# Kernel tuning notes

Measured on AMD Instinct MI355X. Metric: run time of the kernel, lower is better.

## Reference

```python
import jax, jax.numpy as jnp
import numpy as np

D_MODEL = 512
N_HEAD = 8
D_FF = 2048
HEAD = D_MODEL // N_HEAD
B, S = 2, 4096
LN_EPS = 1e-5


def _layernorm(x, g, b):
    mu = jnp.mean(x, axis=-1, keepdims=True)
    var = jnp.mean(jnp.square(x - mu), axis=-1, keepdims=True)
    return (x - mu) * jax.lax.rsqrt(var + LN_EPS) * g + b


def setup_inputs() -> dict:
    key = jax.random.key(0)
    ks = jax.random.split(key, 12)
    s = 0.02
    inp = {
        "src": jax.random.normal(ks[0], (B, S, D_MODEL), dtype=jnp.float32),
        "mask": jnp.ones((B, S, S), dtype=jnp.float32),
        "Wq": jax.random.normal(ks[1], (D_MODEL, D_MODEL), dtype=jnp.float32) * s,
        "bq": jnp.zeros((D_MODEL,), dtype=jnp.float32),
        "Wk": jax.random.normal(ks[2], (D_MODEL, D_MODEL), dtype=jnp.float32) * s,
        "bk": jnp.zeros((D_MODEL,), dtype=jnp.float32),
        "Wv": jax.random.normal(ks[3], (D_MODEL, D_MODEL), dtype=jnp.float32) * s,
        "bv": jnp.zeros((D_MODEL,), dtype=jnp.float32),
        "Wo": jax.random.normal(ks[4], (D_MODEL, D_MODEL), dtype=jnp.float32) * s,
        "bo": jnp.zeros((D_MODEL,), dtype=jnp.float32),
        "W1": jax.random.normal(ks[5], (D_FF, D_MODEL), dtype=jnp.float32) * s,
        "b1": jnp.zeros((D_FF,), dtype=jnp.float32),
        "W2": jax.random.normal(ks[6], (D_MODEL, D_FF), dtype=jnp.float32) * s,
        "b2": jnp.zeros((D_MODEL,), dtype=jnp.float32),
        "ln1_g": jnp.ones((D_MODEL,), dtype=jnp.float32),
        "ln1_b": jnp.zeros((D_MODEL,), dtype=jnp.float32),
        "ln2_g": jnp.ones((D_MODEL,), dtype=jnp.float32),
        "ln2_b": jnp.zeros((D_MODEL,), dtype=jnp.float32),
    }
    return inp


def reference(src, mask, Wq, bq, Wk, bk, Wv, bv, Wo, bo, W1, b1, W2, b2,
              ln1_g, ln1_b, ln2_g, ln2_b):
    # --- multi-head self-attention (chunk/cat == head split on last dim) ---
    def heads(x, W, b):
        y = x @ W.T + b  # [B,S,D]
        return y.reshape(B, S, N_HEAD, HEAD)
    Q = heads(src, Wq, bq)
    K = heads(src, Wk, bk)
    V = heads(src, Wv, bv)
    score = jnp.einsum('bihd,bjhd->bhij', Q, K) / jnp.sqrt(jnp.float32(HEAD))
    score = score + ((1.0 - mask) * -1e9)[:, None, :, :]
    attn = jax.nn.softmax(score, axis=-1)
    ctx = jnp.einsum('bhij,bjhd->bihd', attn, V).reshape(B, S, D_MODEL)
    sa = ctx @ Wo.T + bo
    # --- residual + LN1 ---
    x = _layernorm(src + sa, ln1_g, ln1_b)
    # --- FFN (relu) + residual + LN2 ---
    ff = jax.nn.relu(x @ W1.T + b1) @ W2.T + b2
    return _layernorm(x + ff, ln2_g, ln2_b)
```

## Files before the change

### kernel.cpp

```cpp
#include <hip/hip_runtime.h>
#include <cstdint>
#include <cstddef>

#define DM   512
#define SQL  4096
#define NHE  8
#define HDM  64
#define DFF  2048
#define NB   2

typedef unsigned short u16t;
typedef __attribute__((ext_vector_type(8))) __bf16 bf16x8;
typedef __attribute__((ext_vector_type(4))) float f32x4;
typedef __attribute__((ext_vector_type(8))) unsigned short us8;
typedef __attribute__((ext_vector_type(4))) unsigned short us4;

__device__ inline f32x4 mfma16(bf16x8 a, bf16x8 b, f32x4 c) {
    return __builtin_amdgcn_mfma_f32_16x16x32_bf16(a, b, c, 0, 0, 0);
}

__device__ inline void load_lds16(const void* g, void* l) {
    __builtin_amdgcn_global_load_lds(
        (const __attribute__((address_space(1))) unsigned int*)g,
        (__attribute__((address_space(3))) unsigned int*)l, 16, 0, 0);
}

__device__ inline u16t f2bf(float x) {
    union { float f; unsigned int u; } v; v.f = x;
    unsigned int r = v.u + 0x7fffu + ((v.u >> 16) & 1u);
    return (u16t)(r >> 16);
}

__device__ inline void store_out(float* C, size_t idx, float v) { C[idx] = v; }
__device__ inline void store_out(u16t* C, size_t idx, float v) { C[idx] = f2bf(v); }

__global__ __launch_bounds__(256) void convert_all(
    const float* __restrict__ src, const float* __restrict__ Wq,
    const float* __restrict__ Wk, const float* __restrict__ Wv,
    const float* __restrict__ Wo, const float* __restrict__ W1,
    const float* __restrict__ W2, const float* __restrict__ bq,
    const float* __restrict__ bk, const float* __restrict__ bv,
    u16t* __restrict__ srcbf, u16t* __restrict__ wqkv, u16t* __restrict__ woc,
    u16t* __restrict__ w1c, u16t* __restrict__ w2c,
    float* __restrict__ bqkv, int* __restrict__ flag) {
    const int blk = blockIdx.x;
    const float* s;
    u16t* d;
    int base;
    if (blk < 2048)      { s = src; d = srcbf;           base = blk; }
    else if (blk < 2176) { s = Wq;  d = wqkv;            base = blk - 2048; }
    else if (blk < 2304) { s = Wk;  d = wqkv + 262144;   base = blk - 2176; }
    else if (blk < 2432) { s = Wv;  d = wqkv + 524288;   base = blk - 2304; }
    else if (blk < 2560) { s = Wo;  d = woc;             base = blk - 2432; }
    else if (blk < 3072) { s = W1;  d = w1c;             base = blk - 2560; }
    else if (blk < 3584) { s = W2;  d = w2c;             base = blk - 3072; }
    else {
        for (int i = threadIdx.x; i < 1536; i += 256)
            bqkv[i] = (i < 512) ? bq[i] : (i < 1024 ? bk[i - 512] : bv[i - 1024]);
        if (threadIdx.x == 0) flag[0] = 1;
        return;
    }
    const int i = base * 2048 + threadIdx.x * 8;
    f32x4 a = *(const f32x4*)(s + i);
    f32x4 b = *(const f32x4*)(s + i + 4);
    us8 o;
    o[0] = f2bf(a[0]); o[1] = f2bf(a[1]); o[2] = f2bf(a[2]); o[3] = f2bf(a[3]);
    o[4] = f2bf(b[0]); o[5] = f2bf(b[1]); o[6] = f2bf(b[2]); o[7] = f2bf(b[3]);
    *(us8*)(d + i) = o;
}

__global__ __launch_bounds__(256) void check_mask_k(const f32x4* __restrict__ m, int* flag) {
    const size_t n4 = (size_t)NB * SQL * SQL / 4;
    size_t i = (size_t)blockIdx.x * 256 + threadIdx.x;
    bool bad = false;
    for (; i < n4; i += (size_t)gridDim.x * 256) {
        f32x4 v = m[i];
        bad |= (v[0] != 1.0f) || (v[1] != 1.0f) || (v[2] != 1.0f) || (v[3] != 1.0f);
    }
    if (bad) flag[0] = 0;
}

template <typename OutT, bool RELU>
__global__ __launch_bounds__(256, 3) void gemm_bt(const u16t* __restrict__ A,
                                                  const u16t* __restrict__ Bw,
                                                  const float* __restrict__ bias,
                                                  OutT* __restrict__ C,
                                                  const int M, const int N, const int K,
                                                  const int ldc) {
    __shared__ u16t As[128 * 32];
    __shared__ u16t Bs[128 * 32];
    const int tid = threadIdx.x;
    const int w = tid >> 6, lane = tid & 63;
    const int l15 = lane & 15, quad = lane >> 4;
    const int m0 = blockIdx.y * 128, n0 = blockIdx.x * 128;
    const int wm = w >> 1, wn = w & 1;

    f32x4 acc[4][4] = {};

    const u16t* Ag = A + ((size_t)(m0 + w * 32 + (lane >> 2))) * K + (lane & 3) * 8;
    const u16t* Bg = Bw + ((size_t)(n0 + w * 32 + (lane >> 2))) * K + (lane & 3) * 8;
    u16t* Asw = &As[(w * 32) * 32];
    u16t* Bsw = &Bs[(w * 32) * 32];

    for (int k0 = 0; k0 < K; k0 += 32) {
        __syncthreads();
        load_lds16(Ag + k0, Asw);
        load_lds16(Ag + (size_t)16 * K + k0, Asw + 16 * 32);
        load_lds16(Bg + k0, Bsw);
        load_lds16(Bg + (size_t)16 * K + k0, Bsw + 16 * 32);
        __syncthreads();
        bf16x8 af[4], bfr[4];
#pragma unroll
        for (int mt = 0; mt < 4; ++mt)
            af[mt] = *(const bf16x8*)&As[(wm * 64 + mt * 16 + l15) * 32 + quad * 8];
#pragma unroll
        for (int nt = 0; nt < 4; ++nt)
            bfr[nt] = *(const bf16x8*)&Bs[(wn * 64 + nt * 16 + l15) * 32 + quad * 8];
#pragma unroll
        for (int mt = 0; mt < 4; ++mt)
#pragma unroll
            for (int nt = 0; nt < 4; ++nt)
                acc[mt][nt] = mfma16(af[mt], bfr[nt], acc[mt][nt]);
    }

    float bv[4];
#pragma unroll
    for (int nt = 0; nt < 4; ++nt) bv[nt] = bias[n0 + wn * 64 + nt * 16 + l15];
#pragma unroll
    for (int mt = 0; mt < 4; ++mt)
#pragma unroll
        for (int r = 0; r < 4; ++r) {
            const int row = m0 + wm * 64 + mt * 16 + quad * 4 + r;
#pragma unroll
            for (int nt = 0; nt < 4; ++nt) {
                float v = acc[mt][nt][r] + bv[nt];
                if (RELU) v = fmaxf(v, 0.0f);
                store_out(C, (size_t)row * ldc + n0 + wn * 64 + nt * 16 + l15, v);
            }
        }
}

__global__ __launch_bounds__(256) void transpose_v(const u16t* __restrict__ qkv,
                                                   u16t* __restrict__ vt) {
    __shared__ u16t t[64 * 72];
    const int sb = blockIdx.x, h = blockIdx.y, b = blockIdx.z;
    const int tid = threadIdx.x;
#pragma unroll
    for (int it = 0; it < 2; ++it) {
        const int idx = it * 256 + tid;
        const int r = idx >> 3, c8 = idx & 7;
        const u16t* gp = qkv + (size_t)(b * SQL + sb * 64 + r) * (3 * DM) + 2 * DM + h * HDM + c8 * 8;
        *(us8*)&t[r * 72 + c8 * 8] = *(const us8*)gp;
    }
    __syncthreads();
#pragma unroll
    for (int it = 0; it < 2; ++it) {
        const int idx = it * 256 + tid;
        const int d = idx >> 3, s8 = idx & 7;
        us8 o;
#pragma unroll
        for (int u = 0; u < 8; ++u) o[u] = t[(s8 * 8 + u) * 72 + d];
        u16t* gp = vt + (size_t)((b * NHE + h) * HDM + d) * SQL + sb * 64 + s8 * 8;
        *(us8*)gp = o;
    }
}

__global__ __launch_bounds__(256, 2) void flash_attn(const u16t* __restrict__ qkv,
                                                     const u16t* __restrict__ vtg,
                                                     const float* __restrict__ mask,
                                                     const int* __restrict__ flag,
                                                     u16t* __restrict__ ctx) {
    __shared__ u16t Ks[128 * 64];
    __shared__ u16t Vs[64 * 128];
    __shared__ u16t Ps[4][32 * 128];

    const int qt = blockIdx.x, h = blockIdx.y, b = blockIdx.z;
    const int tid = threadIdx.x;
    const int w = tid >> 6, lane = tid & 63;
    const int l15 = lane & 15, quad = lane >> 4;
    const int e3 = l15 & 7;
    const bool allones = (*flag != 0);

    bf16x8 qf[2][2];
#pragma unroll
    for (int mt = 0; mt < 2; ++mt) {
        const size_t rowb = (size_t)(b * SQL + qt * 128 + w * 32 + mt * 16 + l15) * (3 * DM) + h * HDM;
#pragma unroll
        for (int kk = 0; kk < 2; ++kk)
            qf[mt][kk] = *(const bf16x8*)(qkv + rowb + kk * 32 + quad * 8);
    }

    f32x4 oacc[4][2] = {};
    float m_r[2] = {-3.0e38f, -3.0e38f};
    float l_r[2] = {0.0f, 0.0f};

    const int r8 = lane >> 3, c8 = lane & 7;
    const int r4 = lane >> 4, c16 = lane & 15;

    for (int kt = 0; kt < SQL / 128; ++kt) {
        const int j0 = kt * 128;
        __syncthreads();
#pragma unroll
        for (int i = 0; i < 4; ++i) {
            const int row = j0 + w * 32 + i * 8 + r8;
            load_lds16(qkv + (size_t)(b * SQL + row) * (3 * DM) + DM + h * HDM + ((c8 ^ r8) * 8),
                       &Ks[(w * 32 + i * 8) * 64]);
        }
#pragma unroll
        for (int i = 0; i < 4; ++i) {
            const int d = w * 16 + i * 4 + r4;
            load_lds16(vtg + (size_t)((b * NHE + h) * HDM + d) * SQL + j0 + ((c16 ^ ((i * 4 + r4) & 7)) * 8),
                       &Vs[(w * 16 + i * 4) * 128]);
        }
        __syncthreads();

        f32x4 sacc[2][8] = {};
#pragma unroll
        for (int kk = 0; kk < 2; ++kk) {
#pragma unroll
            for (int jt = 0; jt < 8; ++jt) {
                bf16x8 af = *(const bf16x8*)&Ks[(jt * 16 + l15) * 64 + (((kk * 4 + quad) ^ e3) * 8)];
                sacc[0][jt] = mfma16(af, qf[0][kk], sacc[0][jt]);
                sacc[1][jt] = mfma16(af, qf[1][kk], sacc[1][jt]);
            }
        }

#pragma unroll
        for (int mt = 0; mt < 2; ++mt) {
            float mx = -3.0e38f;
            if (allones) {
#pragma unroll
                for (int jt = 0; jt < 8; ++jt)
#pragma unroll
                    for (int r = 0; r < 4; ++r) {
                        const float v = sacc[mt][jt][r] * 0.125f;
                        sacc[mt][jt][r] = v;
                        mx = fmaxf(mx, v);
                    }
            } else {
                const int gi = qt * 128 + w * 32 + mt * 16 + l15;
#pragma unroll
                for (int jt = 0; jt < 8; ++jt)
#pragma unroll
                    for (int r = 0; r < 4; ++r) {
                        const int gj = j0 + jt * 16 + quad * 4 + r;
                        const float v = sacc[mt][jt][r] * 0.125f
                                      + (1.0f - mask[((size_t)b * SQL + gi) * SQL + gj]) * (-1.0e9f);
                        sacc[mt][jt][r] = v;
                        mx = fmaxf(mx, v);
                    }
            }
            mx = fmaxf(mx, __shfl_xor(mx, 16));
            mx = fmaxf(mx, __shfl_xor(mx, 32));
            const float mnew = fmaxf(m_r[mt], mx);
            const float alpha = __expf(m_r[mt] - mnew);
            m_r[mt] = mnew;
            float rsum = 0.0f;
#pragma unroll
            for (int jt = 0; jt < 8; ++jt) {
                us4 pk;
#pragma unroll
                for (int r = 0; r < 4; ++r) {
                    const float p = __expf(sacc[mt][jt][r] - mnew);
                    rsum += p;
                    pk[r] = f2bf(p);
                }
                *(us4*)&Ps[w][(mt * 16 + l15) * 128
                              + (((jt * 2 + (quad >> 1)) ^ e3) * 8) + (quad & 1) * 4] = pk;
            }
            rsum += __shfl_xor(rsum, 16);
            rsum += __shfl_xor(rsum, 32);
            l_r[mt] = l_r[mt] * alpha + rsum;
#pragma unroll
            for (int dt = 0; dt < 4; ++dt)
#pragma unroll
                for (int r = 0; r < 4; ++r) oacc[dt][mt][r] *= alpha;
        }

#pragma unroll
        for (int ks = 0; ks < 4; ++ks) {
            const int pc = ((ks * 4 + quad) ^ e3) * 8;
            bf16x8 pb0 = *(const bf16x8*)&Ps[w][(l15) * 128 + pc];
            bf16x8 pb1 = *(const bf16x8*)&Ps[w][(16 + l15) * 128 + pc];
#pragma unroll
            for (int dt = 0; dt < 4; ++dt) {
                bf16x8 av = *(const bf16x8*)&Vs[(dt * 16 + l15) * 128 + pc];
                oacc[dt][0] = mfma16(av, pb0, oacc[dt][0]);
                oacc[dt][1] = mfma16(av, pb1, oacc[dt][1]);
            }
        }
    }

#pragma unroll
    for (int mt = 0; mt < 2; ++mt) {
        const float inv = 1.0f / l_r[mt];
        const int token = qt * 128 + w * 32 + mt * 16 + l15;
#pragma unroll
        for (int dt = 0; dt < 4; ++dt) {
            us4 o;
#pragma unroll
            for (int r = 0; r < 4; ++r) o[r] = f2bf(oacc[dt][mt][r] * inv);
            *(us4*)&ctx[(size_t)(b * SQL + token) * DM + h * HDM + dt * 16 + quad * 4] = o;
        }
    }
}

template <bool WBF>
__global__ __launch_bounds__(256) void ln_fused(const float* __restrict__ xa,
                                                const float* __restrict__ xb,
                                                const float* __restrict__ g,
                                                const float* __restrict__ be,
                                                float* __restrict__ outf,
                                                u16t* __restrict__ outh) {
    const int row = blockIdx.x * 4 + (threadIdx.x >> 6);
    const int lane = threadIdx.x & 63;
    const size_t base = (size_t)row * DM;
    f32x4 a0 = *(const f32x4*)(xa + base + lane * 4);
    f32x4 b0 = *(const f32x4*)(xb + base + lane * 4);
    f32x4 a1 = *(const f32x4*)(xa + base + 256 + lane * 4);
    f32x4 b1 = *(const f32x4*)(xb + base + 256 + lane * 4);
    f32x4 v0 = a0 + b0, v1 = a1 + b1;
    float s = v0[0] + v0[1] + v0[2] + v0[3] + v1[0] + v1[1] + v1[2] + v1[3];
    float q = v0[0]*v0[0] + v0[1]*v0[1] + v0[2]*v0[2] + v0[3]*v0[3]
            + v1[0]*v1[0] + v1[1]*v1[1] + v1[2]*v1[2] + v1[3]*v1[3];
#pragma unroll
    for (int off = 1; off < 64; off <<= 1) {
        s += __shfl_xor(s, off);
        q += __shfl_xor(q, off);
    }
    const float mean = s * (1.0f / DM);
    const float var = q * (1.0f / DM) - mean * mean;
    const float rs = rsqrtf(var + 1e-5f);
    f32x4 g0 = *(const f32x4*)(g + lane * 4);
    f32x4 g1 = *(const f32x4*)(g + 256 + lane * 4);
    f32x4 e0 = *(const f32x4*)(be + lane * 4);
    f32x4 e1 = *(const f32x4*)(be + 256 + lane * 4);
    f32x4 y0, y1;
#pragma unroll
    for (int i = 0; i < 4; ++i) {
        y0[i] = (v0[i] - mean) * rs * g0[i] + e0[i];
        y1[i] = (v1[i] - mean) * rs * g1[i] + e1[i];
    }
    *(f32x4*)(outf + base + lane * 4) = y0;
    *(f32x4*)(outf + base + 256 + lane * 4) = y1;
    if (WBF) {
        us4 h0, h1;
#pragma unroll
        for (int i = 0; i < 4; ++i) { h0[i] = f2bf(y0[i]); h1[i] = f2bf(y1[i]); }
        *(us4*)(outh + base + lane * 4) = h0;
        *(us4*)(outh + base + 256 + lane * 4) = h1;
    }
}

extern "C" void kernel_launch(void* const* d_in, const int* in_sizes, int n_in,
                              void* d_out, int out_size, void* d_ws, size_t ws_size,
                              hipStream_t stream) {
    const float* src  = (const float*)d_in[0];
    const float* mask = (const float*)d_in[1];
    const float* Wq = (const float*)d_in[2];
    const float* bq = (const float*)d_in[3];
    const float* Wk = (const float*)d_in[4];
    const float* bk = (const float*)d_in[5];
    const float* Wv = (const float*)d_in[6];
    const float* bv = (const float*)d_in[7];
    const float* Wo = (const float*)d_in[8];
    const float* bo = (const float*)d_in[9];
    const float* W1 = (const float*)d_in[10];
    const float* b1 = (const float*)d_in[11];
    const float* W2 = (const float*)d_in[12];
    const float* b2 = (const float*)d_in[13];
    const float* ln1g = (const float*)d_in[14];
    const float* ln1b = (const float*)d_in[15];
    const float* ln2g = (const float*)d_in[16];
    const float* ln2b = (const float*)d_in[17];

    const int M = NB * SQL;

    char* p = (char*)d_ws;
    auto take = [&](size_t bytes) {
        char* r = p;
        p += (bytes + 1023) & ~(size_t)1023;
        return r;
    };
    u16t* regA   = (u16t*)take((size_t)M * DFF * 2);
    u16t* vtb    = (u16t*)take((size_t)NB * NHE * HDM * SQL * 2);
    u16t* ctxb   = (u16t*)take((size_t)M * DM * 2);
    float* sa_ff = (float*)take((size_t)M * DM * 4);
    float* x1f   = (float*)take((size_t)M * DM * 4);
    u16t* x1h    = (u16t*)take((size_t)M * DM * 2);
    u16t* srcbf  = (u16t*)take((size_t)M * DM * 2);
    u16t* wqkv   = (u16t*)take((size_t)3 * DM * DM * 2);
    float* bqkv  = (float*)take((size_t)3 * DM * 4);
    u16t* woc    = (u16t*)take((size_t)DM * DM * 2);
    u16t* w1c    = (u16t*)take((size_t)DFF * DM * 2);
    u16t* w2c    = (u16t*)take((size_t)DM * DFF * 2);
    int* flag    = (int*)take(1024);
    u16t* qkvb   = regA;
    u16t* hbuf   = regA;

    convert_all<<<3585, 256, 0, stream>>>(src, Wq, Wk, Wv, Wo, W1, W2, bq, bk, bv,
                                          srcbf, wqkv, woc, w1c, w2c, bqkv, flag);
    check_mask_k<<<4096, 256, 0, stream>>>((const f32x4*)mask, flag);

    gemm_bt<u16t, false><<<dim3(12, 64), 256, 0, stream>>>(srcbf, wqkv, bqkv, qkvb,
                                                           M, 3 * DM, DM, 3 * DM);
    transpose_v<<<dim3(SQL / 64, NHE, NB), 256, 0, stream>>>(qkvb, vtb);
    flash_attn<<<dim3(SQL / 128, NHE, NB), 256, 0, stream>>>(qkvb, vtb, mask, flag, ctxb);
    gemm_bt<float, false><<<dim3(4, 64), 256, 0, stream>>>(ctxb, woc, bo, sa_ff,
                                                           M, DM, DM, DM);
    ln_fused<true><<<M / 4, 256, 0, stream>>>(src, sa_ff, ln1g, ln1b, x1f, x1h);
    gemm_bt<u16t, true><<<dim3(16, 64), 256, 0, stream>>>(x1h, w1c, b1, hbuf,
                                                          M, DFF, DM, DFF);
    gemm_bt<float, false><<<dim3(4, 64), 256, 0, stream>>>(hbuf, w2c, b2, sa_ff,
                                                           M, DM, DFF, DM);
    ln_fused<false><<<M / 4, 256, 0, stream>>>(x1f, sa_ff, ln2g, ln2b, (float*)d_out,
                                               (u16t*)nullptr);
}
```

Measured before the change: 497.2 us.

## Keep softmax probabilities in registers and feed PV MFMA directly, drop LDS P buffer

The attention kernel no longer writes the bf16 probabilities to a per-wave LDS scratch and reads them back. The S accumulator layout is reused directly as the A operand of a 16x16x16 bf16 MFMA, with V and O roles transposed and per-row alpha and l values redistributed by shuffles. Dropping the P buffer frees LDS so occupancy is raised to 4 blocks per CU, and the scale and exp are folded into a single exp2 with a premultiplied constant. In exchange the PV product uses the narrower K=16 MFMA (twice as many instructions), the output stores become scalar 2-byte writes, and the higher occupancy target may cause register spills.

Measured after the change: 738.4 us. 1.49x slower.

```diff
diff --git a/kernel.cpp b/kernel.cpp
--- a/kernel.cpp
+++ b/kernel.cpp
@@ -14,9 +14,13 @@
 typedef __attribute__((ext_vector_type(4))) float f32x4;
 typedef __attribute__((ext_vector_type(8))) unsigned short us8;
 typedef __attribute__((ext_vector_type(4))) unsigned short us4;
+typedef __attribute__((ext_vector_type(4))) short s16x4;
 
 __device__ inline f32x4 mfma16(bf16x8 a, bf16x8 b, f32x4 c) {
     return __builtin_amdgcn_mfma_f32_16x16x32_bf16(a, b, c, 0, 0, 0);
+}
+__device__ inline f32x4 mfma16k16(s16x4 a, s16x4 b, f32x4 c) {
+    return __builtin_amdgcn_mfma_f32_16x16x16bf16_1k(a, b, c, 0, 0, 0);
 }
 
 __device__ inline void load_lds16(const void* g, void* l) {
@@ -165,14 +169,13 @@
     }
 }
 
-__global__ __launch_bounds__(256, 2) void flash_attn(const u16t* __restrict__ qkv,
+__global__ __launch_bounds__(256, 4) void flash_attn(const u16t* __restrict__ qkv,
                                                      const u16t* __restrict__ vtg,
                                                      const float* __restrict__ mask,
                                                      const int* __restrict__ flag,
                                                      u16t* __restrict__ ctx) {
     __shared__ u16t Ks[128 * 64];
     __shared__ u16t Vs[64 * 128];
-    __shared__ u16t Ps[4][32 * 128];
 
     const int qt = blockIdx.x, h = blockIdx.y, b = blockIdx.z;
     const int tid = threadIdx.x;
@@ -225,82 +228,83 @@
             }
         }
 
+        float av[2][4];
 #pragma unroll
         for (int mt = 0; mt < 2; ++mt) {
-            float mx = -3.0e38f;
-            if (allones) {
-#pragma unroll
-                for (int jt = 0; jt < 8; ++jt)
-#pragma unroll
-                    for (int r = 0; r < 4; ++r) {
-                        const float v = sacc[mt][jt][r] * 0.125f;
-                        sacc[mt][jt][r] = v;
-                        mx = fmaxf(mx, v);
-                    }
-            } else {
+            if (!allones) {
                 const int gi = qt * 128 + w * 32 + mt * 16 + l15;
 #pragma unroll
                 for (int jt = 0; jt < 8; ++jt)
 #pragma unroll
                     for (int r = 0; r < 4; ++r) {
                         const int gj = j0 + jt * 16 + quad * 4 + r;
-                        const float v = sacc[mt][jt][r] * 0.125f
-                                      + (1.0f - mask[((size_t)b * SQL + gi) * SQL + gj]) * (-1.0e9f);
-                        sacc[mt][jt][r] = v;
-                        mx = fmaxf(mx, v);
+                        sacc[mt][jt][r] = sacc[mt][jt][r] * 0.125f
+                                        + (1.0f - mask[((size_t)b * SQL + gi) * SQL + gj]) * (-1.0e9f);
                     }
             }
+            float mx = -3.0e38f;
+#pragma unroll
+            for (int jt = 0; jt < 8; ++jt)
+#pragma unroll
+                for (int r = 0; r < 4; ++r) mx = fmaxf(mx, sacc[mt][jt][r]);
             mx = fmaxf(mx, __shfl_xor(mx, 16));
             mx = fmaxf(mx, __shfl_xor(mx, 32));
+            const float cs = allones ? 0.18033688011112042f : 1.4426950408889634f;
             const float mnew = fmaxf(m_r[mt], mx);
-            const float alpha = __expf(m_r[mt] - mnew);
+            const float mb = mnew * cs;
+            const float alpha = exp2f(fmaf(m_r[mt], cs, -mb));
             m_r[mt] = mnew;
             float rsum = 0.0f;
 #pragma unroll
-            for (int jt = 0; jt < 8; ++jt) {
-                us4 pk;
+            for (int jt = 0; jt < 8; ++jt)
 #pragma unroll
                 for (int r = 0; r < 4; ++r) {
-                    const float p = __expf(sacc[mt][jt][r] - mnew);
+                    const float p = exp2f(fmaf(sacc[mt][jt][r], cs, -mb));
+                    sacc[mt][jt][r] = p;
                     rsum += p;
-                    pk[r] = f2bf(p);
                 }
-                *(us4*)&Ps[w][(mt * 16 + l15) * 128
-                              + (((jt * 2 + (quad >> 1)) ^ e3) * 8) + (quad & 1) * 4] = pk;
-            }
             rsum += __shfl_xor(rsum, 16);
             rsum += __shfl_xor(rsum, 32);
             l_r[mt] = l_r[mt] * alpha + rsum;
 #pragma unroll
+            for (int r = 0; r < 4; ++r) av[mt][r] = __shfl(alpha, quad * 4 + r);
+#pragma unroll
             for (int dt = 0; dt < 4; ++dt)
 #pragma unroll
-                for (int r = 0; r < 4; ++r) oacc[dt][mt][r] *= alpha;
-        }
-
-#pragma unroll
-        for (int ks = 0; ks < 4; ++ks) {
-            const int pc = ((ks * 4 + quad) ^ e3) * 8;
-            bf16x8 pb0 = *(const bf16x8*)&Ps[w][(l15) * 128 + pc];
-            bf16x8 pb1 = *(const bf16x8*)&Ps[w][(16 + l15) * 128 + pc];
+                for (int r = 0; r < 4; ++r) oacc[dt][mt][r] *= av[mt][r];
+        }
+
+#pragma unroll
+        for (int jt = 0; jt < 8; ++jt) {
+            s16x4 pa0, pa1;
+#pragma unroll
+            for (int r = 0; r < 4; ++r) {
+                pa0[r] = (short)f2bf(sacc[0][jt][r]);
+                pa1[r] = (short)f2bf(sacc[1][jt][r]);
+            }
+            const int vcol = (((2 * jt + (quad >> 1)) ^ e3) * 8) + (quad & 1) * 4;
 #pragma unroll
             for (int dt = 0; dt < 4; ++dt) {
-                bf16x8 av = *(const bf16x8*)&Vs[(dt * 16 + l15) * 128 + pc];
-                oacc[dt][0] = mfma16(av, pb0, oacc[dt][0]);
-                oacc[dt][1] = mfma16(av, pb1, oacc[dt][1]);
+                s16x4 vb = *(const s16x4*)&Vs[(dt * 16 + l15) * 128 + vcol];
+                oacc[dt][0] = mfma16k16(pa0, vb, oacc[dt][0]);
+                oacc[dt][1] = mfma16k16(pa1, vb, oacc[dt][1]);
             }
         }
     }
 
 #pragma unroll
     for (int mt = 0; mt < 2; ++mt) {
-        const float inv = 1.0f / l_r[mt];
-        const int token = qt * 128 + w * 32 + mt * 16 + l15;
-#pragma unroll
-        for (int dt = 0; dt < 4; ++dt) {
-            us4 o;
-#pragma unroll
-            for (int r = 0; r < 4; ++r) o[r] = f2bf(oacc[dt][mt][r] * inv);
-            *(us4*)&ctx[(size_t)(b * SQL + token) * DM + h * HDM + dt * 16 + quad * 4] = o;
+        float lv[4];
+#pragma unroll
+        for (int r = 0; r < 4; ++r) lv[r] = __shfl(l_r[mt], quad * 4 + r);
+#pragma unroll
+        for (int r = 0; r < 4; ++r) {
+            const float inv = 1.0f / lv[r];
+            const int token = qt * 128 + w * 32 + mt * 16 + quad * 4 + r;
+            const size_t base = (size_t)(b * SQL + token) * DM + h * HDM;
+#pragma unroll
+            for (int dt = 0; dt < 4; ++dt)
+                ctx[base + dt * 16 + l15] = f2bf(oacc[dt][mt][r] * inv);
         }
     }
 }
```
